# Optimization experiments

Measured on AMD Instinct MI355X. Metric: run time of the kernel, lower is better.

The kernel has to match this reference:

```python
import jax, jax.numpy as jnp
import numpy as np
from math import sqrt

N, D = 8192, 64

def setup_inputs() -> dict:
    key = jax.random.key(0)
    kq, kk, kv = jax.random.split(key, 3)
    q = jax.random.normal(kq, (N, D), dtype=jnp.float32)
    k = jax.random.normal(kk, (N, D), dtype=jnp.float32)
    v = jax.random.normal(kv, (N, D), dtype=jnp.float32)
    return {"q": q, "k": k, "v": v}

def reference(q, k, v):
    # Mathematically identical to the block-wise online-softmax loop:
    # after processing all KV blocks, m_blk == rowmax(S), l_blk == rowsum(exp(S - m)),
    # O = (exp(S - m) @ V) / l.
    scale = 1.0 / sqrt(q.shape[-1])
    S = (q @ k.T) * scale            # [N, N] attention scores
    m = jnp.max(S, axis=1, keepdims=True)   # running max -> global row max
    P = jnp.exp(S - m)                      # unnormalized probs
    L = jnp.sum(P, axis=1, keepdims=True)   # softmax denominator, [N, 1]
    O = (P @ v) / L                          # [N, D]
    return (O, L)
```

## Files before the change

kernel.cpp:

```cpp
#include <hip/hip_runtime.h>
#include <hip/hip_bf16.h>
#include <math.h>

#define N 8192
#define D 64
#define QSCALE 0.18033688011112042f

typedef __attribute__((ext_vector_type(8))) short short8;
typedef __attribute__((ext_vector_type(16))) float f32x16;
typedef __attribute__((ext_vector_type(4))) unsigned int ui4;

__device__ inline short f32_to_bf16_bits(float x) {
    unsigned u = __builtin_bit_cast(unsigned, x);
    u += 0x7FFFu + ((u >> 16) & 1u);
    return (short)(u >> 16);
}
__device__ inline float bfbits_to_f32(unsigned short u) {
    return __builtin_bit_cast(float, ((unsigned)u) << 16);
}
__device__ inline unsigned cvt_pk_bf16(float a, float b) {
    unsigned r;
    asm("v_cvt_pk_bf16_f32 %0, %1, %2" : "=v"(r) : "v"(a), "v"(b));
    return r;
}
__device__ inline float max3f(float a, float b, float c) {
    float d;
    asm("v_max3_f32 %0, %1, %2, %3" : "=v"(d) : "v"(a), "v"(b), "v"(c));
    return d;
}

__global__ __launch_bounds__(256) void fa_conv(const float* __restrict__ q,
                                               const float* __restrict__ k,
                                               const float* __restrict__ v,
                                               short* __restrict__ Qb,
                                               short* __restrict__ Kp,
                                               short* __restrict__ Vp) {
    int bid = blockIdx.x, tid = threadIdx.x;
    if (bid < 512) {
        int i = (bid * 256 + tid) * 4;
        float4 a = *(const float4*)(q + i);
        unsigned lo = cvt_pk_bf16(a.x * QSCALE, a.y * QSCALE);
        unsigned hi = cvt_pk_bf16(a.z * QSCALE, a.w * QSCALE);
        unsigned long long u = (unsigned long long)lo | ((unsigned long long)hi << 32);
        *(unsigned long long*)(Qb + i) = u;
    } else if (bid < 768) {
        int t = bid - 512;
        int c = tid >> 6, l = tid & 63, ql = l & 31, hi = l >> 5;
        const float* src = k + (size_t)(t * 32 + ql) * D + c * 16 + hi * 8;
        float4 a = *(const float4*)(src);
        float4 b = *(const float4*)(src + 4);
        uint4 u = { cvt_pk_bf16(a.x, a.y), cvt_pk_bf16(a.z, a.w),
                    cvt_pk_bf16(b.x, b.y), cvt_pk_bf16(b.z, b.w) };
        *(uint4*)(Kp + (size_t)t * 2048 + c * 512 + l * 8) = u;
    } else {
        int t = bid - 768;
        int dt = tid >> 7, h = (tid >> 6) & 1, hi = (tid >> 5) & 1, ql = tid & 31;
        const float* src = v + (size_t)(t * 32 + h * 16 + hi * 4) * D + dt * 32 + ql;
        float f[8];
#pragma unroll
        for (int j = 0; j < 8; ++j)
            f[j] = src[(size_t)((j & 3) + 8 * (j >> 2)) * D];
        uint4 u = { cvt_pk_bf16(f[0], f[1]), cvt_pk_bf16(f[2], f[3]),
                    cvt_pk_bf16(f[4], f[5]), cvt_pk_bf16(f[6], f[7]) };
        *(uint4*)(Vp + (size_t)t * 2048 + dt * 1024 + h * 512 + hi * 256 + ql * 8) = u;
    }
}

__global__ __launch_bounds__(256) void fa_part_kernel(const short* __restrict__ Qb,
                                                      const short* __restrict__ Kp,
                                                      const short* __restrict__ Vp,
                                                      short* __restrict__ OTb,
                                                      float* __restrict__ Ml,
                                                      int KN) {
    const int s  = blockIdx.x & 15;
    const int qt = blockIdx.x >> 4;
    const int w = threadIdx.x >> 6, lane = threadIdx.x & 63;
    const int ql = lane & 31, hi = lane >> 5;
    const int qrow = qt * 128 + w * 32 + ql;

    const short* qp = Qb + (size_t)qrow * D + hi * 8;
    short8 qf0 = *(const short8*)(qp);
    short8 qf1 = *(const short8*)(qp + 16);
    short8 qf2 = *(const short8*)(qp + 32);
    short8 qf3 = *(const short8*)(qp + 48);

    f32x16 acc0 = {}, acc1 = {};
    float mex = -INFINITY, lsum = 0.f;

    const int t0 = (s * KN) >> 5, nt = KN >> 5;
    const short* kp = Kp + (size_t)t0 * 2048 + lane * 8;
    const short* vp = Vp + (size_t)t0 * 2048 + lane * 8;

    short8 kA0, kA1, kA2, kA3, kB0, kB1, kB2, kB3;
    short8 vA0, vA1, vA2, vA3, vB0, vB1, vB2, vB3;

#define LOADK(d0, d1, d2, d3) do {                                         \
        d0 = *(const short8*)(kp);                                         \
        d1 = *(const short8*)(kp + 512);                                   \
        d2 = *(const short8*)(kp + 1024);                                  \
        d3 = *(const short8*)(kp + 1536);                                  \
        kp += 2048;                                                        \
    } while (0)
#define LOADV(d0, d1, d2, d3) do {                                         \
        d0 = *(const short8*)(vp);                                         \
        d1 = *(const short8*)(vp + 512);                                   \
        d2 = *(const short8*)(vp + 1024);                                  \
        d3 = *(const short8*)(vp + 1536);                                  \
        vp += 2048;                                                        \
    } while (0)

#define TILE(K0, K1, K2, K3, V0, V1, V2, V3) do {                           \
        f32x16 st = {};                                                     \
        st = __builtin_amdgcn_mfma_f32_32x32x16_bf16(K0, qf0, st, 0, 0, 0); \
        st = __builtin_amdgcn_mfma_f32_32x32x16_bf16(K1, qf1, st, 0, 0, 0); \
        st = __builtin_amdgcn_mfma_f32_32x32x16_bf16(K2, qf2, st, 0, 0, 0); \
        st = __builtin_amdgcn_mfma_f32_32x32x16_bf16(K3, qf3, st, 0, 0, 0); \
        float m0_ = max3f(st[0], st[1], st[2]);                             \
        float m1_ = max3f(st[3], st[4], st[5]);                             \
        float m2_ = max3f(st[6], st[7], st[8]);                             \
        float m3_ = max3f(st[9], st[10], st[11]);                           \
        float m4_ = max3f(st[12], st[13], st[14]);                          \
        mex = max3f(mex, max3f(m0_, m1_, m2_), max3f(m3_, m4_, st[15]));    \
        unsigned pk0, pk1, pk2, pk3, pk4, pk5, pk6, pk7;                    \
        float rs_;                                                          \
        {                                                                   \
            float a_, b_;                                                   \
            a_ = __builtin_amdgcn_exp2f(st[0]);  b_ = __builtin_amdgcn_exp2f(st[1]);  \
            rs_ = a_ + b_;         pk0 = cvt_pk_bf16(a_, b_);               \
            a_ = __builtin_amdgcn_exp2f(st[2]);  b_ = __builtin_amdgcn_exp2f(st[3]);  \
            rs_ += a_ + b_;        pk1 = cvt_pk_bf16(a_, b_);               \
            a_ = __builtin_amdgcn_exp2f(st[4]);  b_ = __builtin_amdgcn_exp2f(st[5]);  \
            rs_ += a_ + b_;        pk2 = cvt_pk_bf16(a_, b_);               \
            a_ = __builtin_amdgcn_exp2f(st[6]);  b_ = __builtin_amdgcn_exp2f(st[7]);  \
            rs_ += a_ + b_;        pk3 = cvt_pk_bf16(a_, b_);               \
            a_ = __builtin_amdgcn_exp2f(st[8]);  b_ = __builtin_amdgcn_exp2f(st[9]);  \
            rs_ += a_ + b_;        pk4 = cvt_pk_bf16(a_, b_);               \
            a_ = __builtin_amdgcn_exp2f(st[10]); b_ = __builtin_amdgcn_exp2f(st[11]); \
            rs_ += a_ + b_;        pk5 = cvt_pk_bf16(a_, b_);               \
            a_ = __builtin_amdgcn_exp2f(st[12]); b_ = __builtin_amdgcn_exp2f(st[13]); \
            rs_ += a_ + b_;        pk6 = cvt_pk_bf16(a_, b_);               \
            a_ = __builtin_amdgcn_exp2f(st[14]); b_ = __builtin_amdgcn_exp2f(st[15]); \
            rs_ += a_ + b_;        pk7 = cvt_pk_bf16(a_, b_);               \
        }                                                                   \
        lsum += rs_;                                                        \
        ui4 va_ = { pk0, pk1, pk2, pk3 };                                   \
        ui4 vb_ = { pk4, pk5, pk6, pk7 };                                   \
        short8 pb0 = __builtin_bit_cast(short8, va_);                       \
        short8 pb1 = __builtin_bit_cast(short8, vb_);                       \
        acc0 = __builtin_amdgcn_mfma_f32_32x32x16_bf16(V0, pb0, acc0, 0, 0, 0); \
        acc0 = __builtin_amdgcn_mfma_f32_32x32x16_bf16(V1, pb1, acc0, 0, 0, 0); \
        acc1 = __builtin_amdgcn_mfma_f32_32x32x16_bf16(V2, pb0, acc1, 0, 0, 0); \
        acc1 = __builtin_amdgcn_mfma_f32_32x32x16_bf16(V3, pb1, acc1, 0, 0, 0); \
    } while (0)

    LOADK(kA0, kA1, kA2, kA3);
    LOADV(vA0, vA1, vA2, vA3);
#pragma unroll 1
    for (int T = 0; T < nt; T += 2) {
        LOADK(kB0, kB1, kB2, kB3);
        LOADV(vB0, vB1, vB2, vB3);
        TILE(kA0, kA1, kA2, kA3, vA0, vA1, vA2, vA3);
        if (T + 2 < nt) {
            LOADK(kA0, kA1, kA2, kA3);
            LOADV(vA0, vA1, vA2, vA3);
        }
        TILE(kB0, kB1, kB2, kB3, vB0, vB1, vB2, vB3);
    }
#undef LOADK
#undef LOADV
#undef TILE

    mex = fmaxf(mex, __shfl_xor(mex, 32));
    lsum += __shfl_xor(lsum, 32);

#pragma unroll
    for (int r = 0; r < 16; ++r) {
        int d0 = (r & 3) + 8 * (r >> 2) + 4 * hi;
        OTb[(size_t)(s * 64 + d0) * N + qrow]      = f32_to_bf16_bits(acc0[r]);
        OTb[(size_t)(s * 64 + 32 + d0) * N + qrow] = f32_to_bf16_bits(acc1[r]);
    }
    if (hi == 0) {
        Ml[(size_t)(s * 2 + 0) * N + qrow] = lsum;
        Ml[(size_t)(s * 2 + 1) * N + qrow] = mex;
    }
}

__global__ __launch_bounds__(256) void fa_comb_kernel(const short* __restrict__ OTb,
                                                      const float* __restrict__ Ml,
                                                      float* __restrict__ Out, int S) {
    const int qb = blockIdx.x >> 2, db4 = blockIdx.x & 3;
    const int row = threadIdx.x & 63, dd = threadIdx.x >> 6;
    const int grow = qb * 64 + row;
    const int d0 = db4 * 16 + dd * 4;

    float v0 = 0.f, v1 = 0.f, v2 = 0.f, v3 = 0.f;
    float L = 0.f, mg = -INFINITY;
    for (int s = 0; s < S; ++s) {
        size_t base = (size_t)(s * 64 + d0) * N + grow;
        v0 += bfbits_to_f32((unsigned short)OTb[base]);
        v1 += bfbits_to_f32((unsigned short)OTb[base + (size_t)N]);
        v2 += bfbits_to_f32((unsigned short)OTb[base + (size_t)2 * N]);
        v3 += bfbits_to_f32((unsigned short)OTb[base + (size_t)3 * N]);
        L  += Ml[(size_t)(s * 2 + 0) * N + grow];
        mg = fmaxf(mg, Ml[(size_t)(s * 2 + 1) * N + grow]);
    }
    float inv = 1.0f / L;
    float4 o = { v0 * inv, v1 * inv, v2 * inv, v3 * inv };
    *(float4*)(Out + (size_t)grow * D + d0) = o;
    if (db4 == 0 && dd == 0) Out[(size_t)N * D + grow] = exp2f(-mg) * L;
}

extern "C" void kernel_launch(void* const* d_in, const int* in_sizes, int n_in,
                              void* d_out, int out_size, void* d_ws, size_t ws_size,
                              hipStream_t stream) {
    const float* q = (const float*)d_in[0];
    const float* k = (const float*)d_in[1];
    const float* v = (const float*)d_in[2];
    float* out = (float*)d_out;

    short* Qb = (short*)d_ws;
    short* Kp = Qb + (size_t)N * D;
    short* Vp = Kp + (size_t)N * D;
    short* OTb = (short*)((char*)d_ws + 3 * 1048576);

    int S = 16;
    while (S > 1 &&
           3ull * 1048576 + (size_t)S * (64ull * N * 2) + (size_t)S * (2ull * N * 4) > ws_size)
        S >>= 1;
    float* Ml = (float*)(OTb + (size_t)S * 64 * N);
    int KN = N / S;

    fa_conv<<<1024, 256, 0, stream>>>(q, k, v, Qb, Kp, Vp);
    fa_part_kernel<<<64 * S, 256, 0, stream>>>(Qb, Kp, Vp, OTb, Ml, KN);
    fa_comb_kernel<<<(N / 64) * 4, 256, 0, stream>>>(OTb, Ml, out, S);
}
```

Baseline: 45.36 us.

## Interleave QK and PV MFMAs, transpose V via LDS, reorder block mapping

The inner loop is reordered so the second tile's QK matmul is issued before the first tile's PV matmul, letting the matrix units overlap with the exp/softmax math. The V conversion now loads coalesced rows into a shared-memory tile and transposes there instead of doing strided global loads. The block index mapping changes so adjacent blocks share the same KV split rather than the same query tile, which alters L2 reuse of K/V. The interleaving keeps more score values live and raises register pressure.

```diff
diff --git a/kernel.cpp b/kernel.cpp
--- a/kernel.cpp
+++ b/kernel.cpp
@@ -35,6 +35,7 @@
                                                short* __restrict__ Qb,
                                                short* __restrict__ Kp,
                                                short* __restrict__ Vp) {
+    __shared__ short tile[32][72];
     int bid = blockIdx.x, tid = threadIdx.x;
     if (bid < 512) {
         int i = (bid * 256 + tid) * 4;
@@ -54,16 +55,83 @@
         *(uint4*)(Kp + (size_t)t * 2048 + c * 512 + l * 8) = u;
     } else {
         int t = bid - 768;
-        int dt = tid >> 7, h = (tid >> 6) & 1, hi = (tid >> 5) & 1, ql = tid & 31;
-        const float* src = v + (size_t)(t * 32 + h * 16 + hi * 4) * D + dt * 32 + ql;
-        float f[8];
+        {
+            int r = tid >> 3, c0 = (tid & 7) * 8;
+            const float* src = v + (size_t)(t * 32 + r) * D + c0;
+            float4 a = *(const float4*)(src);
+            float4 b = *(const float4*)(src + 4);
+            ui4 u = { cvt_pk_bf16(a.x, a.y), cvt_pk_bf16(a.z, a.w),
+                      cvt_pk_bf16(b.x, b.y), cvt_pk_bf16(b.z, b.w) };
+            *(ui4*)(&tile[r][c0]) = u;
+        }
+        __syncthreads();
+        int dt = tid >> 7, h = (tid >> 6) & 1, h3 = (tid >> 5) & 1, vq = tid & 31;
+        int col = dt * 32 + vq;
+        unsigned short e[8];
 #pragma unroll
-        for (int j = 0; j < 8; ++j)
-            f[j] = src[(size_t)((j & 3) + 8 * (j >> 2)) * D];
-        uint4 u = { cvt_pk_bf16(f[0], f[1]), cvt_pk_bf16(f[2], f[3]),
-                    cvt_pk_bf16(f[4], f[5]), cvt_pk_bf16(f[6], f[7]) };
-        *(uint4*)(Vp + (size_t)t * 2048 + dt * 1024 + h * 512 + hi * 256 + ql * 8) = u;
-    }
+        for (int j = 0; j < 8; ++j) {
+            int kl = h * 16 + h3 * 4 + (j & 3) + 8 * (j >> 2);
+            e[j] = (unsigned short)tile[kl][col];
+        }
+        ui4 u = { (unsigned)e[0] | ((unsigned)e[1] << 16),
+                  (unsigned)e[2] | ((unsigned)e[3] << 16),
+                  (unsigned)e[4] | ((unsigned)e[5] << 16),
+                  (unsigned)e[6] | ((unsigned)e[7] << 16) };
+        *(ui4*)(Vp + (size_t)t * 2048 + dt * 1024 + h * 512 + h3 * 256 + vq * 8) = u;
+    }
+}
+
+__device__ inline f32x16 qk4(short8 K0, short8 K1, short8 K2, short8 K3,
+                             short8 qf0, short8 qf1, short8 qf2, short8 qf3) {
+    f32x16 st = {};
+    st = __builtin_amdgcn_mfma_f32_32x32x16_bf16(K0, qf0, st, 0, 0, 0);
+    st = __builtin_amdgcn_mfma_f32_32x32x16_bf16(K1, qf1, st, 0, 0, 0);
+    st = __builtin_amdgcn_mfma_f32_32x32x16_bf16(K2, qf2, st, 0, 0, 0);
+    st = __builtin_amdgcn_mfma_f32_32x32x16_bf16(K3, qf3, st, 0, 0, 0);
+    return st;
+}
+__device__ inline void sm_phase(const f32x16 st, short8& pb0, short8& pb1,
+                                float& mex, float& lsum) {
+    float m0 = max3f(st[0], st[1], st[2]);
+    float m1 = max3f(st[3], st[4], st[5]);
+    float m2 = max3f(st[6], st[7], st[8]);
+    float m3 = max3f(st[9], st[10], st[11]);
+    float m4 = max3f(st[12], st[13], st[14]);
+    mex = max3f(mex, max3f(m0, m1, m2), max3f(m3, m4, st[15]));
+    unsigned pk0, pk1, pk2, pk3, pk4, pk5, pk6, pk7;
+    float rs;
+    {
+        float a, b;
+        a = __builtin_amdgcn_exp2f(st[0]);  b = __builtin_amdgcn_exp2f(st[1]);
+        rs = a + b;    pk0 = cvt_pk_bf16(a, b);
+        a = __builtin_amdgcn_exp2f(st[2]);  b = __builtin_amdgcn_exp2f(st[3]);
+        rs += a + b;   pk1 = cvt_pk_bf16(a, b);
+        a = __builtin_amdgcn_exp2f(st[4]);  b = __builtin_amdgcn_exp2f(st[5]);
+        rs += a + b;   pk2 = cvt_pk_bf16(a, b);
+        a = __builtin_amdgcn_exp2f(st[6]);  b = __builtin_amdgcn_exp2f(st[7]);
+        rs += a + b;   pk3 = cvt_pk_bf16(a, b);
+        a = __builtin_amdgcn_exp2f(st[8]);  b = __builtin_amdgcn_exp2f(st[9]);
+        rs += a + b;   pk4 = cvt_pk_bf16(a, b);
+        a = __builtin_amdgcn_exp2f(st[10]); b = __builtin_amdgcn_exp2f(st[11]);
+        rs += a + b;   pk5 = cvt_pk_bf16(a, b);
+        a = __builtin_amdgcn_exp2f(st[12]); b = __builtin_amdgcn_exp2f(st[13]);
+        rs += a + b;   pk6 = cvt_pk_bf16(a, b);
+        a = __builtin_amdgcn_exp2f(st[14]); b = __builtin_amdgcn_exp2f(st[15]);
+        rs += a + b;   pk7 = cvt_pk_bf16(a, b);
+    }
+    lsum += rs;
+    ui4 va = { pk0, pk1, pk2, pk3 };
+    ui4 vb = { pk4, pk5, pk6, pk7 };
+    pb0 = __builtin_bit_cast(short8, va);
+    pb1 = __builtin_bit_cast(short8, vb);
+}
+__device__ inline void pv4(f32x16& acc0, f32x16& acc1,
+                           short8 V0, short8 V1, short8 V2, short8 V3,
+                           short8 pb0, short8 pb1) {
+    acc0 = __builtin_amdgcn_mfma_f32_32x32x16_bf16(V0, pb0, acc0, 0, 0, 0);
+    acc0 = __builtin_amdgcn_mfma_f32_32x32x16_bf16(V1, pb1, acc0, 0, 0, 0);
+    acc1 = __builtin_amdgcn_mfma_f32_32x32x16_bf16(V2, pb0, acc1, 0, 0, 0);
+    acc1 = __builtin_amdgcn_mfma_f32_32x32x16_bf16(V3, pb1, acc1, 0, 0, 0);
 }
 
 __global__ __launch_bounds__(256) void fa_part_kernel(const short* __restrict__ Qb,
@@ -72,8 +140,8 @@
                                                       short* __restrict__ OTb,
                                                       float* __restrict__ Ml,
                                                       int KN) {
-    const int s  = blockIdx.x & 15;
-    const int qt = blockIdx.x >> 4;
+    const int qt = blockIdx.x & 63;
+    const int s  = blockIdx.x >> 6;
     const int w = threadIdx.x >> 6, lane = threadIdx.x & 63;
     const int ql = lane & 31, hi = lane >> 5;
     const int qrow = qt * 128 + w * 32 + ql;
@@ -109,66 +177,27 @@
         vp += 2048;                                                        \
     } while (0)
 
-#define TILE(K0, K1, K2, K3, V0, V1, V2, V3) do {                           \
-        f32x16 st = {};                                                     \
-        st = __builtin_amdgcn_mfma_f32_32x32x16_bf16(K0, qf0, st, 0, 0, 0); \
-        st = __builtin_amdgcn_mfma_f32_32x32x16_bf16(K1, qf1, st, 0, 0, 0); \
-        st = __builtin_amdgcn_mfma_f32_32x32x16_bf16(K2, qf2, st, 0, 0, 0); \
-        st = __builtin_amdgcn_mfma_f32_32x32x16_bf16(K3, qf3, st, 0, 0, 0); \
-        float m0_ = max3f(st[0], st[1], st[2]);                             \
-        float m1_ = max3f(st[3], st[4], st[5]);                             \
-        float m2_ = max3f(st[6], st[7], st[8]);                             \
-        float m3_ = max3f(st[9], st[10], st[11]);                           \
-        float m4_ = max3f(st[12], st[13], st[14]);                          \
-        mex = max3f(mex, max3f(m0_, m1_, m2_), max3f(m3_, m4_, st[15]));    \
-        unsigned pk0, pk1, pk2, pk3, pk4, pk5, pk6, pk7;                    \
-        float rs_;                                                          \
-        {                                                                   \
-            float a_, b_;                                                   \
-            a_ = __builtin_amdgcn_exp2f(st[0]);  b_ = __builtin_amdgcn_exp2f(st[1]);  \
-            rs_ = a_ + b_;         pk0 = cvt_pk_bf16(a_, b_);               \
-            a_ = __builtin_amdgcn_exp2f(st[2]);  b_ = __builtin_amdgcn_exp2f(st[3]);  \
-            rs_ += a_ + b_;        pk1 = cvt_pk_bf16(a_, b_);               \
-            a_ = __builtin_amdgcn_exp2f(st[4]);  b_ = __builtin_amdgcn_exp2f(st[5]);  \
-            rs_ += a_ + b_;        pk2 = cvt_pk_bf16(a_, b_);               \
-            a_ = __builtin_amdgcn_exp2f(st[6]);  b_ = __builtin_amdgcn_exp2f(st[7]);  \
-            rs_ += a_ + b_;        pk3 = cvt_pk_bf16(a_, b_);               \
-            a_ = __builtin_amdgcn_exp2f(st[8]);  b_ = __builtin_amdgcn_exp2f(st[9]);  \
-            rs_ += a_ + b_;        pk4 = cvt_pk_bf16(a_, b_);               \
-            a_ = __builtin_amdgcn_exp2f(st[10]); b_ = __builtin_amdgcn_exp2f(st[11]); \
-            rs_ += a_ + b_;        pk5 = cvt_pk_bf16(a_, b_);               \
-            a_ = __builtin_amdgcn_exp2f(st[12]); b_ = __builtin_amdgcn_exp2f(st[13]); \
-            rs_ += a_ + b_;        pk6 = cvt_pk_bf16(a_, b_);               \
-            a_ = __builtin_amdgcn_exp2f(st[14]); b_ = __builtin_amdgcn_exp2f(st[15]); \
-            rs_ += a_ + b_;        pk7 = cvt_pk_bf16(a_, b_);               \
-        }                                                                   \
-        lsum += rs_;                                                        \
-        ui4 va_ = { pk0, pk1, pk2, pk3 };                                   \
-        ui4 vb_ = { pk4, pk5, pk6, pk7 };                                   \
-        short8 pb0 = __builtin_bit_cast(short8, va_);                       \
-        short8 pb1 = __builtin_bit_cast(short8, vb_);                       \
-        acc0 = __builtin_amdgcn_mfma_f32_32x32x16_bf16(V0, pb0, acc0, 0, 0, 0); \
-        acc0 = __builtin_amdgcn_mfma_f32_32x32x16_bf16(V1, pb1, acc0, 0, 0, 0); \
-        acc1 = __builtin_amdgcn_mfma_f32_32x32x16_bf16(V2, pb0, acc1, 0, 0, 0); \
-        acc1 = __builtin_amdgcn_mfma_f32_32x32x16_bf16(V3, pb1, acc1, 0, 0, 0); \
-    } while (0)
-
     LOADK(kA0, kA1, kA2, kA3);
     LOADV(vA0, vA1, vA2, vA3);
 #pragma unroll 1
     for (int T = 0; T < nt; T += 2) {
         LOADK(kB0, kB1, kB2, kB3);
         LOADV(vB0, vB1, vB2, vB3);
-        TILE(kA0, kA1, kA2, kA3, vA0, vA1, vA2, vA3);
+        f32x16 stA = qk4(kA0, kA1, kA2, kA3, qf0, qf1, qf2, qf3);
+        short8 pbA0, pbA1;
+        sm_phase(stA, pbA0, pbA1, mex, lsum);
+        f32x16 stB = qk4(kB0, kB1, kB2, kB3, qf0, qf1, qf2, qf3);
+        pv4(acc0, acc1, vA0, vA1, vA2, vA3, pbA0, pbA1);
         if (T + 2 < nt) {
             LOADK(kA0, kA1, kA2, kA3);
             LOADV(vA0, vA1, vA2, vA3);
         }
-        TILE(kB0, kB1, kB2, kB3, vB0, vB1, vB2, vB3);
+        short8 pbB0, pbB1;
+        sm_phase(stB, pbB0, pbB1, mex, lsum);
+        pv4(acc0, acc1, vB0, vB1, vB2, vB3, pbB0, pbB1);
     }
 #undef LOADK
 #undef LOADV
-#undef TILE
 
     mex = fmaxf(mex, __shfl_xor(mex, 32));
     lsum += __shfl_xor(lsum, 32);
```

Result: no change. 46.26 us (+2.0%).
